# Kernel optimization log

Measured on AMD Instinct MI355X. Metric: run time of the kernel, lower is better.

The kernel has to match this reference:

```python
import jax, jax.numpy as jnp
import numpy as np

N = 3072      # atoms
C_A = 128     # atom channel
C_S = 384     # style/cond channel
C_Z = 16      # pair channel
H = 4         # heads
D = C_A // H  # head dim = 32
NEXP = 2      # FFN expansion
BIASINIT = -2.0


def _ln(x, eps=1e-5):
    m = x.mean(-1, keepdims=True)
    v = x.var(-1, keepdims=True)
    return (x - m) * jax.lax.rsqrt(v + eps)


def _adaln(a, s, s_w, scale_w, scale_b, shift_w):
    # AF3 Algorithm 26: a<-LN(a,no affine); s<-LN(s,no offset); a<-sigmoid(Lin(s))*a + LinNoBias(s)
    an = _ln(a)
    sn = _ln(s) * s_w
    return jax.nn.sigmoid(sn @ scale_w + scale_b) * an + sn @ shift_w


def setup_inputs() -> dict:
    key = jax.random.key(0)
    ks = iter(jax.random.split(key, 40))
    def w(shape, scale=0.02):
        return jax.random.normal(next(ks), shape, jnp.float32) * scale
    inp = dict(
        a=jax.random.normal(next(ks), (N, C_A), jnp.float32),
        s=jax.random.normal(next(ks), (N, C_S), jnp.float32),
        z=jax.random.normal(next(ks), (N, N, C_Z), jnp.float32),
        # AttentionPairBias: AdaLN params
        aln1_s_w=jnp.ones((C_S,), jnp.float32),
        aln1_scale_w=w((C_S, C_A)), aln1_scale_b=jnp.zeros((C_A,), jnp.float32),
        aln1_shift_w=w((C_S, C_A)),
        # attention projections
        wq=w((C_A, C_A)), bq=jnp.zeros((C_A,), jnp.float32),
        wk=w((C_A, C_A)), wv=w((C_A, C_A)),
        ln_z_w=jnp.ones((C_Z,), jnp.float32), ln_z_b=jnp.zeros((C_Z,), jnp.float32),
        wb=w((C_Z, H)),
        wg=w((C_A, C_A)), wo=w((C_A, C_A)),
        sgate1_w=w((C_S, C_A)), sgate1_b=jnp.full((C_A,), BIASINIT, jnp.float32),
        # ConditionedTransitionBlock: AdaLN params
        aln2_s_w=jnp.ones((C_S,), jnp.float32),
        aln2_scale_w=w((C_S, C_A)), aln2_scale_b=jnp.zeros((C_A,), jnp.float32),
        aln2_shift_w=w((C_S, C_A)),
        # SwiGLU FFN
        w1=w((C_A, NEXP * C_A)), w2=w((C_A, NEXP * C_A)), wout=w((NEXP * C_A, C_A)),
        sgate2_w=w((C_S, C_A)), sgate2_b=jnp.full((C_A,), BIASINIT, jnp.float32),
    )
    return inp


def reference(a, s, z,
              aln1_s_w, aln1_scale_w, aln1_scale_b, aln1_shift_w,
              wq, bq, wk, wv, ln_z_w, ln_z_b, wb, wg, wo, sgate1_w, sgate1_b,
              aln2_s_w, aln2_scale_w, aln2_scale_b, aln2_shift_w,
              w1, w2, wout, sgate2_w, sgate2_b):
    # ---- AttentionPairBias (Alg 24) ----
    h = _adaln(a, s, aln1_s_w, aln1_scale_w, aln1_scale_b, aln1_shift_w)
    q = (h @ wq + bq).reshape(N, H, D)
    k = (h @ wk).reshape(N, H, D)
    v = (h @ wv).reshape(N, H, D)
    # pair bias from layernormed z: [N, N, H]
    bias = (_ln(z) * ln_z_w + ln_z_b) @ wb
    logits = jnp.einsum('qhd,khd->hqk', q, k) / np.float32(np.sqrt(D)) + bias.transpose(2, 0, 1)
    attnw = jax.nn.softmax(logits, axis=-1)
    o = jnp.einsum('hqk,khd->qhd', attnw, v)
    g = jax.nn.sigmoid(h @ wg).reshape(N, H, D)
    attn = (g * o).reshape(N, C_A) @ wo
    attn = jax.nn.sigmoid(s @ sgate1_w + sgate1_b) * attn
    attn_out = attn + a  # residual 1
    # ---- ConditionedTransitionBlock (Alg 25) ----
    h2 = _adaln(attn_out, s, aln2_s_w, aln2_scale_w, aln2_scale_b, aln2_shift_w)
    gated = jax.nn.silu(h2 @ w1) * (h2 @ w2)  # SwiGLU, [N, 2*C_A]
    ff = jax.nn.sigmoid(s @ sgate2_w + sgate2_b) * (gated @ wout)
    out_a = ff + attn_out  # residual 2
    return out_a
```

## Files before the change

kernel.cpp:

```cpp
#include <hip/hip_runtime.h>
#include <math.h>

#define N_ATOMS 3072
#define C_Ac 128
#define C_Sc 384
#define C_Zc 16
#define QT 64
#define KC 16
#define CHUNK (N_ATOMS/KC)
#define KT 8
#define NST (CHUNK/KT)
#define NQT (N_ATOMS/QT)

__device__ __forceinline__ float sigm(float x){ return 1.f/(1.f+__expf(-x)); }

__global__ __launch_bounds__(256) void k_stage_a(
    const float* __restrict__ a, const float* __restrict__ s,
    const float* __restrict__ s_w, const float* __restrict__ scale_w,
    const float* __restrict__ scale_b, const float* __restrict__ shift_w,
    const float* __restrict__ wq, const float* __restrict__ bq,
    const float* __restrict__ wk, const float* __restrict__ wv,
    const float* __restrict__ wg,
    float* __restrict__ qo, float* __restrict__ ko, float* __restrict__ vo,
    float* __restrict__ go, float* __restrict__ lns)
{
  __shared__ float sn[4][C_Sc];
  __shared__ float an[4][C_Ac];
  __shared__ float hsh[4][C_Ac];
  __shared__ float t1[4][C_Ac], t2[4][C_Ac];
  int n0 = blockIdx.x*4;
  int tid = threadIdx.x, w = tid>>6, lane = tid&63;

  {
    const float* srow = s + (size_t)(n0+w)*C_Sc;
    float v[6]; float sx=0.f, sxx=0.f;
    #pragma unroll
    for (int j=0;j<6;j++){ v[j]=srow[lane+j*64]; sx+=v[j]; sxx+=v[j]*v[j]; }
    #pragma unroll
    for (int off=32;off;off>>=1){ sx+=__shfl_xor(sx,off,64); sxx+=__shfl_xor(sxx,off,64); }
    float mean=sx*(1.f/C_Sc), rs=rsqrtf(sxx*(1.f/C_Sc)-mean*mean+1e-5f);
    #pragma unroll
    for (int j=0;j<6;j++){
      int i=lane+j*64;
      float ln=(v[j]-mean)*rs;
      lns[(size_t)(n0+w)*C_Sc+i]=ln;
      sn[w][i]=ln*s_w[i];
    }
  }
  {
    const float* arow = a + (size_t)(n0+w)*C_Ac;
    float v0=arow[lane], v1=arow[lane+64];
    float sx=v0+v1, sxx=v0*v0+v1*v1;
    #pragma unroll
    for (int off=32;off;off>>=1){ sx+=__shfl_xor(sx,off,64); sxx+=__shfl_xor(sxx,off,64); }
    float mean=sx*(1.f/C_Ac), rs=rsqrtf(sxx*(1.f/C_Ac)-mean*mean+1e-5f);
    an[w][lane]=(v0-mean)*rs; an[w][lane+64]=(v1-mean)*rs;
  }
  __syncthreads();

  {
    int c = tid&127, sel = tid>>7;
    const float* W = sel ? shift_w : scale_w;
    float acc[4];
    #pragma unroll
    for (int r=0;r<4;r++) acc[r] = sel ? 0.f : scale_b[c];
    for (int i=0;i<C_Sc;i++){
      float wv = W[(size_t)i*C_Ac+c];
      #pragma unroll
      for (int r=0;r<4;r++) acc[r] += sn[r][i]*wv;
    }
    if (sel==0){ t1[0][c]=sigm(acc[0]); t1[1][c]=sigm(acc[1]); t1[2][c]=sigm(acc[2]); t1[3][c]=sigm(acc[3]); }
    else       { t2[0][c]=acc[0]; t2[1][c]=acc[1]; t2[2][c]=acc[2]; t2[3][c]=acc[3]; }
  }
  __syncthreads();
  for (int f=tid; f<512; f+=256){ int r=f>>7, c=f&127; hsh[r][c] = t1[r][c]*an[r][c] + t2[r][c]; }
  __syncthreads();

  {
    int c = tid&127, sel = tid>>7;
    const float* Wa = sel ? wv : wq;
    const float* Wb = sel ? wg : wk;
    float accA[4], accB[4];
    #pragma unroll
    for (int r=0;r<4;r++){ accA[r] = sel ? 0.f : bq[c]; accB[r]=0.f; }
    for (int i=0;i<C_Ac;i++){
      float wa=Wa[(size_t)i*C_Ac+c], wb_=Wb[(size_t)i*C_Ac+c];
      #pragma unroll
      for (int r=0;r<4;r++){ float hv=hsh[r][i]; accA[r]+=hv*wa; accB[r]+=hv*wb_; }
    }
    #pragma unroll
    for (int r=0;r<4;r++){
      size_t idx = (size_t)(n0+r)*C_Ac + c;
      if (sel==0){ qo[idx]=accA[r]; ko[idx]=accB[r]; }
      else       { vo[idx]=accA[r]; go[idx]=sigm(accB[r]); }
    }
  }
}

__global__ __launch_bounds__(256) void k_attn(
    const float* __restrict__ z, const float* __restrict__ ln_z_w,
    const float* __restrict__ ln_z_b, const float* __restrict__ wb,
    const float* __restrict__ qws, const float* __restrict__ kws,
    const float* __restrict__ vws,
    float* __restrict__ part_m, float* __restrict__ part_l,
    float* __restrict__ part_o)
{
  __shared__ float bias[4][QT][KT+1];
  __shared__ float ks[KT][C_Ac];
  __shared__ float vs[KT][C_Ac];
  __shared__ float lwb_s[C_Zc][4];
  __shared__ float csum_s[4], bb_s[4];

  int qt = blockIdx.x, chunk = blockIdx.y;
  int q0 = qt*QT, k_base = chunk*CHUNK;
  int tid = threadIdx.x, w = tid>>6, lane = tid&63;

  if (tid < 64){ int c = tid>>2, h = tid&3; lwb_s[c][h] = ln_z_w[c]*wb[c*4+h]; }
  if (tid < 4){
    float cs=0.f, bbv=0.f;
    #pragma unroll
    for (int c=0;c<C_Zc;c++){ cs += ln_z_w[c]*wb[c*4+tid]; bbv += ln_z_b[c]*wb[c*4+tid]; }
    csum_s[tid]=cs; bb_s[tid]=bbv;
  }
  __syncthreads();

  float qv[32];
  {
    const float4* qp = (const float4*)(qws + (size_t)(q0+lane)*C_Ac + w*32);
    #pragma unroll
    for (int j=0;j<8;j++){ float4 t=qp[j]; qv[4*j]=t.x; qv[4*j+1]=t.y; qv[4*j+2]=t.z; qv[4*j+3]=t.w; }
  }
  float m=-INFINITY, l=0.f, o[32];
  #pragma unroll
  for (int j=0;j<32;j++) o[j]=0.f;
  const float isd = 0.17677669529663687f;

  float z0[16], z1[16];
  float4 kreg, vreg;
  const int qla = (tid>>3), qlb = 32 + (tid>>3), klz = tid&7;

  {
    int k0n = k_base;
    const float4* zp0 = (const float4*)(z + ((size_t)(q0+qla)*N_ATOMS + (k0n+klz))*C_Zc);
    const float4* zp1 = (const float4*)(z + ((size_t)(q0+qlb)*N_ATOMS + (k0n+klz))*C_Zc);
    #pragma unroll
    for (int j=0;j<4;j++){ float4 t=zp0[j]; z0[4*j]=t.x; z0[4*j+1]=t.y; z0[4*j+2]=t.z; z0[4*j+3]=t.w; }
    #pragma unroll
    for (int j=0;j<4;j++){ float4 t=zp1[j]; z1[4*j]=t.x; z1[4*j+1]=t.y; z1[4*j+2]=t.z; z1[4*j+3]=t.w; }
    kreg = ((const float4*)(kws + (size_t)(k0n + (tid>>5))*C_Ac))[tid&31];
    vreg = ((const float4*)(vws + (size_t)(k0n + (tid>>5))*C_Ac))[tid&31];
  }

  #pragma unroll 1
  for (int st=0; st<NST; st++){
    ((float4*)ks)[tid] = kreg;
    ((float4*)vs)[tid] = vreg;
    {
      float sum=0.f, ssq=0.f;
      #pragma unroll
      for (int c=0;c<16;c++){ sum+=z0[c]; ssq+=z0[c]*z0[c]; }
      float mz=sum*(1.f/16), rz=rsqrtf(ssq*(1.f/16)-mz*mz+1e-5f);
      float d0=0.f,d1=0.f,d2=0.f,d3=0.f;
      #pragma unroll
      for (int c=0;c<16;c++){ float zc=z0[c];
        d0=fmaf(zc,lwb_s[c][0],d0); d1=fmaf(zc,lwb_s[c][1],d1);
        d2=fmaf(zc,lwb_s[c][2],d2); d3=fmaf(zc,lwb_s[c][3],d3); }
      bias[0][qla][klz]=rz*(d0-mz*csum_s[0])+bb_s[0];
      bias[1][qla][klz]=rz*(d1-mz*csum_s[1])+bb_s[1];
      bias[2][qla][klz]=rz*(d2-mz*csum_s[2])+bb_s[2];
      bias[3][qla][klz]=rz*(d3-mz*csum_s[3])+bb_s[3];
    }
    {
      float sum=0.f, ssq=0.f;
      #pragma unroll
      for (int c=0;c<16;c++){ sum+=z1[c]; ssq+=z1[c]*z1[c]; }
      float mz=sum*(1.f/16), rz=rsqrtf(ssq*(1.f/16)-mz*mz+1e-5f);
      float d0=0.f,d1=0.f,d2=0.f,d3=0.f;
      #pragma unroll
      for (int c=0;c<16;c++){ float zc=z1[c];
        d0=fmaf(zc,lwb_s[c][0],d0); d1=fmaf(zc,lwb_s[c][1],d1);
        d2=fmaf(zc,lwb_s[c][2],d2); d3=fmaf(zc,lwb_s[c][3],d3); }
      bias[0][qlb][klz]=rz*(d0-mz*csum_s[0])+bb_s[0];
      bias[1][qlb][klz]=rz*(d1-mz*csum_s[1])+bb_s[1];
      bias[2][qlb][klz]=rz*(d2-mz*csum_s[2])+bb_s[2];
      bias[3][qlb][klz]=rz*(d3-mz*csum_s[3])+bb_s[3];
    }
    if (st+1 < NST){
      int k0n = k_base + (st+1)*KT;
      const float4* zp0 = (const float4*)(z + ((size_t)(q0+qla)*N_ATOMS + (k0n+klz))*C_Zc);
      const float4* zp1 = (const float4*)(z + ((size_t)(q0+qlb)*N_ATOMS + (k0n+klz))*C_Zc);
      #pragma unroll
      for (int j=0;j<4;j++){ float4 t=zp0[j]; z0[4*j]=t.x; z0[4*j+1]=t.y; z0[4*j+2]=t.z; z0[4*j+3]=t.w; }
      #pragma unroll
      for (int j=0;j<4;j++){ float4 t=zp1[j]; z1[4*j]=t.x; z1[4*j+1]=t.y; z1[4*j+2]=t.z; z1[4*j+3]=t.w; }
      kreg = ((const float4*)(kws + (size_t)(k0n + (tid>>5))*C_Ac))[tid&31];
      vreg = ((const float4*)(vws + (size_t)(k0n + (tid>>5))*C_Ac))[tid&31];
    }
    asm volatile("s_waitcnt lgkmcnt(0)" ::: "memory");
    __builtin_amdgcn_s_barrier();
    float lg[KT];
    #pragma unroll
    for (int kl=0;kl<KT;kl++) lg[kl] = bias[w][lane][kl];
    #pragma unroll
    for (int kl=0;kl<KT;kl++){
      const float4* kp = (const float4*)&ks[kl][w*32];
      float d0=0.f,d1=0.f,d2=0.f,d3=0.f;
      #pragma unroll
      for (int j=0;j<8;j++){ float4 t=kp[j];
        d0=fmaf(qv[4*j],t.x,d0); d1=fmaf(qv[4*j+1],t.y,d1);
        d2=fmaf(qv[4*j+2],t.z,d2); d3=fmaf(qv[4*j+3],t.w,d3); }
      lg[kl] = fmaf((d0+d1)+(d2+d3), isd, lg[kl]);
    }
    float tm = fmaxf(fmaxf(fmaxf(lg[0],lg[1]),fmaxf(lg[2],lg[3])),
                     fmaxf(fmaxf(lg[4],lg[5]),fmaxf(lg[6],lg[7])));
    float mn = fmaxf(m, tm);
    float ef = __expf(m-mn);
    float ssum = 0.f;
    #pragma unroll
    for (int kl=0;kl<KT;kl++){ float e=__expf(lg[kl]-mn); lg[kl]=e; ssum+=e; }
    l = l*ef + ssum; m = mn;
    #pragma unroll
    for (int j=0;j<32;j++) o[j]*=ef;
    #pragma unroll
    for (int kl=0;kl<KT;kl++){
      const float4* vp = (const float4*)&vs[kl][w*32];
      float e = lg[kl];
      #pragma unroll
      for (int j=0;j<8;j++){ float4 t=vp[j];
        o[4*j]  =fmaf(e,t.x,o[4*j]);   o[4*j+1]=fmaf(e,t.y,o[4*j+1]);
        o[4*j+2]=fmaf(e,t.z,o[4*j+2]); o[4*j+3]=fmaf(e,t.w,o[4*j+3]); }
    }
    asm volatile("s_waitcnt lgkmcnt(0)" ::: "memory");
    __builtin_amdgcn_s_barrier();
  }

  size_t pb = (((size_t)chunk*NQT + qt)*4 + w)*64 + lane;
  part_m[pb]=m; part_l[pb]=l;
  float4* po = (float4*)(part_o + pb*32);
  #pragma unroll
  for (int j=0;j<8;j++){ po[j] = make_float4(o[4*j],o[4*j+1],o[4*j+2],o[4*j+3]); }
}

__global__ __launch_bounds__(256) void k_combine(
    const float* __restrict__ part_m, const float* __restrict__ part_l,
    const float* __restrict__ part_o, const float* __restrict__ gws,
    float* __restrict__ gows)
{
  int qt = blockIdx.x, h = blockIdx.y;
  int tid = threadIdx.x, ql = tid&63, dg = tid>>6;
  float mc[KC], lc[KC], M=-INFINITY;
  #pragma unroll
  for (int c=0;c<KC;c++){
    size_t pb = (((size_t)c*NQT + qt)*4 + h)*64 + ql;
    mc[c]=part_m[pb]; lc[c]=part_l[pb]; M=fmaxf(M,mc[c]);
  }
  float L=0.f, oa[8];
  #pragma unroll
  for (int j=0;j<8;j++) oa[j]=0.f;
  #pragma unroll
  for (int c=0;c<KC;c++){
    float sc=__expf(mc[c]-M);
    L += lc[c]*sc;
    const float4* po = (const float4*)(part_o + ((((size_t)c*NQT + qt)*4 + h)*64 + ql)*32 + dg*8);
    float4 t0=po[0], t1=po[1];
    oa[0]+=sc*t0.x; oa[1]+=sc*t0.y; oa[2]+=sc*t0.z; oa[3]+=sc*t0.w;
    oa[4]+=sc*t1.x; oa[5]+=sc*t1.y; oa[6]+=sc*t1.z; oa[7]+=sc*t1.w;
  }
  float invL = 1.f/L;
  size_t base = (size_t)(qt*64+ql)*C_Ac + h*32 + dg*8;
  #pragma unroll
  for (int j=0;j<8;j++) gows[base+j] = gws[base+j]*oa[j]*invL;
}

__global__ __launch_bounds__(256) void k_stage_c(
    const float* __restrict__ gows, const float* __restrict__ wo,
    const float* __restrict__ s, const float* __restrict__ sgate1_w,
    const float* __restrict__ sgate1_b, const float* __restrict__ a,
    const float* __restrict__ lns, const float* __restrict__ s_w2,
    const float* __restrict__ scale_w2, const float* __restrict__ scale_b2,
    const float* __restrict__ shift_w2, const float* __restrict__ w1,
    const float* __restrict__ w2, const float* __restrict__ wout,
    const float* __restrict__ sgate2_w, const float* __restrict__ sgate2_b,
    float* __restrict__ out)
{
  __shared__ float srow[4][C_Sc], sn2[4][C_Sc];
  __shared__ float gor[4][C_Ac], ats[4][C_Ac], h2[4][C_Ac];
  __shared__ float gated[4][2*C_Ac];
  __shared__ float t1[4][C_Ac], t2[4][C_Ac], ta[4][C_Ac], tb[4][C_Ac];
  int n0 = blockIdx.x*4;
  int tid = threadIdx.x, w = tid>>6, lane = tid&63;

  for (int r=0;r<4;r++)
    for (int i=tid;i<C_Sc;i+=256){
      float sv = s[(size_t)(n0+r)*C_Sc+i];
      srow[r][i]=sv;
      sn2[r][i]=lns[(size_t)(n0+r)*C_Sc+i]*s_w2[i];
    }
  for (int f=tid; f<512; f+=256){ int r=f>>7, c=f&127; gor[r][c]=gows[(size_t)(n0+r)*C_Ac+c]; }
  __syncthreads();

  {
    int c = tid&127, sel = tid>>7;
    float acc[4];
    if (sel==0){
      #pragma unroll
      for (int r=0;r<4;r++) acc[r]=0.f;
      for (int i=0;i<C_Ac;i++){
        float wv=wo[(size_t)i*C_Ac+c];
        #pragma unroll
        for (int r=0;r<4;r++) acc[r]+=gor[r][i]*wv;
      }
      #pragma unroll
      for (int r=0;r<4;r++) t1[r][c]=acc[r];
    } else {
      #pragma unroll
      for (int r=0;r<4;r++) acc[r]=sgate1_b[c];
      for (int i=0;i<C_Sc;i++){
        float wv=sgate1_w[(size_t)i*C_Ac+c];
        #pragma unroll
        for (int r=0;r<4;r++) acc[r]+=srow[r][i]*wv;
      }
      #pragma unroll
      for (int r=0;r<4;r++) t2[r][c]=sigm(acc[r]);
    }
  }
  __syncthreads();
  for (int f=tid; f<512; f+=256){ int r=f>>7, c=f&127;
    ats[r][c] = t2[r][c]*t1[r][c] + a[(size_t)(n0+r)*C_Ac+c]; }
  __syncthreads();

  {
    float v0=ats[w][lane], v1=ats[w][lane+64];
    float sx=v0+v1, sxx=v0*v0+v1*v1;
    #pragma unroll
    for (int off=32;off;off>>=1){ sx+=__shfl_xor(sx,off,64); sxx+=__shfl_xor(sxx,off,64); }
    float mean=sx*(1.f/C_Ac), rs=rsqrtf(sxx*(1.f/C_Ac)-mean*mean+1e-5f);
    t1[w][lane]=(v0-mean)*rs; t1[w][lane+64]=(v1-mean)*rs;
  }
  __syncthreads();

  {
    int c = tid&127, sel = tid>>7;
    float acc[4];
    const float* W = sel ? shift_w2 : scale_w2;
    #pragma unroll
    for (int r=0;r<4;r++) acc[r] = sel ? 0.f : scale_b2[c];
    for (int i=0;i<C_Sc;i++){
      float wv=W[(size_t)i*C_Ac+c];
      #pragma unroll
      for (int r=0;r<4;r++) acc[r]+=sn2[r][i]*wv;
    }
    if (sel==0){ 
      #pragma unroll
      for (int r=0;r<4;r++) ta[r][c]=sigm(acc[r])*t1[r][c];
    } else {
      #pragma unroll
      for (int r=0;r<4;r++) tb[r][c]=acc[r];
    }
  }
  __syncthreads();
  for (int f=tid; f<512; f+=256){ int r=f>>7, c=f&127; h2[r][c]=ta[r][c]+tb[r][c]; }
  __syncthreads();

  {
    int j = tid;
    float a1[4], a2[4];
    #pragma unroll
    for (int r=0;r<4;r++){ a1[r]=0.f; a2[r]=0.f; }
    for (int i=0;i<C_Ac;i++){
      float w1v=w1[(size_t)i*2*C_Ac+j], w2v=w2[(size_t)i*2*C_Ac+j];
      #pragma unroll
      for (int r=0;r<4;r++){ float hv=h2[r][i]; a1[r]+=hv*w1v; a2[r]+=hv*w2v; }
    }
    #pragma unroll
    for (int r=0;r<4;r++) gated[r][j]=a1[r]*sigm(a1[r])*a2[r];
  }
  __syncthreads();

  {
    int c = tid&127, sel = tid>>7;
    float acc[4];
    if (sel==0){
      #pragma unroll
      for (int r=0;r<4;r++) acc[r]=0.f;
      for (int j=0;j<2*C_Ac;j++){
        float wv=wout[(size_t)j*C_Ac+c];
        #pragma unroll
        for (int r=0;r<4;r++) acc[r]+=gated[r][j]*wv;
      }
      #pragma unroll
      for (int r=0;r<4;r++) t1[r][c]=acc[r];
    } else {
      #pragma unroll
      for (int r=0;r<4;r++) acc[r]=sgate2_b[c];
      for (int i=0;i<C_Sc;i++){
        float wv=sgate2_w[(size_t)i*C_Ac+c];
        #pragma unroll
        for (int r=0;r<4;r++) acc[r]+=srow[r][i]*wv;
      }
      #pragma unroll
      for (int r=0;r<4;r++) t2[r][c]=sigm(acc[r]);
    }
  }
  __syncthreads();
  for (int f=tid; f<512; f+=256){ int r=f>>7, c=f&127;
    out[(size_t)(n0+r)*C_Ac+c] = t2[r][c]*t1[r][c] + ats[r][c]; }
}

extern "C" void kernel_launch(void* const* d_in, const int* in_sizes, int n_in,
                              void* d_out, int out_size, void* d_ws, size_t ws_size,
                              hipStream_t stream)
{
  const float* a            = (const float*)d_in[0];
  const float* s            = (const float*)d_in[1];
  const float* z            = (const float*)d_in[2];
  const float* aln1_s_w     = (const float*)d_in[3];
  const float* aln1_scale_w = (const float*)d_in[4];
  const float* aln1_scale_b = (const float*)d_in[5];
  const float* aln1_shift_w = (const float*)d_in[6];
  const float* wq           = (const float*)d_in[7];
  const float* bq           = (const float*)d_in[8];
  const float* wk           = (const float*)d_in[9];
  const float* wv           = (const float*)d_in[10];
  const float* ln_z_w       = (const float*)d_in[11];
  const float* ln_z_b       = (const float*)d_in[12];
  const float* wb           = (const float*)d_in[13];
  const float* wg           = (const float*)d_in[14];
  const float* wo           = (const float*)d_in[15];
  const float* sgate1_w     = (const float*)d_in[16];
  const float* sgate1_b     = (const float*)d_in[17];
  const float* aln2_s_w     = (const float*)d_in[18];
  const float* aln2_scale_w = (const float*)d_in[19];
  const float* aln2_scale_b = (const float*)d_in[20];
  const float* aln2_shift_w = (const float*)d_in[21];
  const float* w1           = (const float*)d_in[22];
  const float* w2           = (const float*)d_in[23];
  const float* wout         = (const float*)d_in[24];
  const float* sgate2_w     = (const float*)d_in[25];
  const float* sgate2_b     = (const float*)d_in[26];
  float* out = (float*)d_out;

  float* ws   = (float*)d_ws;
  float* qws  = ws;
  float* kws  = qws  + (size_t)N_ATOMS*C_Ac;
  float* vws  = kws  + (size_t)N_ATOMS*C_Ac;
  float* gws  = vws  + (size_t)N_ATOMS*C_Ac;
  float* gows = gws  + (size_t)N_ATOMS*C_Ac;
  float* lns  = gows + (size_t)N_ATOMS*C_Ac;
  float* part_m = lns + (size_t)N_ATOMS*C_Sc;
  float* part_l = part_m + (size_t)KC*NQT*4*64;
  float* part_o = part_l + (size_t)KC*NQT*4*64;

  hipLaunchKernelGGL(k_stage_a, dim3(N_ATOMS/4), dim3(256), 0, stream,
      a, s, aln1_s_w, aln1_scale_w, aln1_scale_b, aln1_shift_w,
      wq, bq, wk, wv, wg, qws, kws, vws, gws, lns);
  hipLaunchKernelGGL(k_attn, dim3(NQT, KC), dim3(256), 0, stream,
      z, ln_z_w, ln_z_b, wb, qws, kws, vws, part_m, part_l, part_o);
  hipLaunchKernelGGL(k_combine, dim3(NQT, 4), dim3(256), 0, stream,
      part_m, part_l, part_o, gws, gows);
  hipLaunchKernelGGL(k_stage_c, dim3(N_ATOMS/4), dim3(256), 0, stream,
      gows, wo, s, sgate1_w, sgate1_b, a, lns, aln2_s_w,
      aln2_scale_w, aln2_scale_b, aln2_shift_w, w1, w2, wout,
      sgate2_w, sgate2_b, out);
}
```

Baseline: 1.108 ms.

## Process 8 rows per block in dense stages and double-buffer attention z prefetch

The pre- and post-attention dense kernels now handle 8 atoms per block instead of 4. Activations are stored transposed in shared memory so each step reads 8 values with float4 loads, which halves weight reloads per output row. The attention kernel gains a second register buffer for z/K/V, prefetching two tiles ahead to hide global load latency, at the cost of more registers and possibly lower occupancy. Stage C reuses one shared pool for all its buffers to keep LDS within limits.

```diff
diff --git a/kernel.cpp b/kernel.cpp
--- a/kernel.cpp
+++ b/kernel.cpp
@@ -24,15 +24,17 @@
     float* __restrict__ qo, float* __restrict__ ko, float* __restrict__ vo,
     float* __restrict__ go, float* __restrict__ lns)
 {
-  __shared__ float sn[4][C_Sc];
-  __shared__ float an[4][C_Ac];
-  __shared__ float hsh[4][C_Ac];
-  __shared__ float t1[4][C_Ac], t2[4][C_Ac];
-  int n0 = blockIdx.x*4;
+  __shared__ __align__(16) float snT[C_Sc][12];
+  __shared__ __align__(16) float an[8][C_Ac];
+  __shared__ __align__(16) float t1[8][C_Ac], t2[8][C_Ac];
+  __shared__ __align__(16) float hshT[C_Ac][12];
+  int n0 = blockIdx.x*8;
   int tid = threadIdx.x, w = tid>>6, lane = tid&63;
 
-  {
-    const float* srow = s + (size_t)(n0+w)*C_Sc;
+  #pragma unroll
+  for (int rr=0; rr<2; rr++){
+    int r = w + rr*4;
+    const float* srow = s + (size_t)(n0+r)*C_Sc;
     float v[6]; float sx=0.f, sxx=0.f;
     #pragma unroll
     for (int j=0;j<6;j++){ v[j]=srow[lane+j*64]; sx+=v[j]; sxx+=v[j]*v[j]; }
@@ -43,56 +45,79 @@
     for (int j=0;j<6;j++){
       int i=lane+j*64;
       float ln=(v[j]-mean)*rs;
-      lns[(size_t)(n0+w)*C_Sc+i]=ln;
-      sn[w][i]=ln*s_w[i];
-    }
-  }
-  {
-    const float* arow = a + (size_t)(n0+w)*C_Ac;
+      lns[(size_t)(n0+r)*C_Sc+i]=ln;
+      snT[i][r]=ln*s_w[i];
+    }
+  }
+  #pragma unroll
+  for (int rr=0; rr<2; rr++){
+    int r = w + rr*4;
+    const float* arow = a + (size_t)(n0+r)*C_Ac;
     float v0=arow[lane], v1=arow[lane+64];
     float sx=v0+v1, sxx=v0*v0+v1*v1;
     #pragma unroll
     for (int off=32;off;off>>=1){ sx+=__shfl_xor(sx,off,64); sxx+=__shfl_xor(sxx,off,64); }
     float mean=sx*(1.f/C_Ac), rs=rsqrtf(sxx*(1.f/C_Ac)-mean*mean+1e-5f);
-    an[w][lane]=(v0-mean)*rs; an[w][lane+64]=(v1-mean)*rs;
+    an[r][lane]=(v0-mean)*rs; an[r][lane+64]=(v1-mean)*rs;
   }
   __syncthreads();
 
   {
     int c = tid&127, sel = tid>>7;
     const float* W = sel ? shift_w : scale_w;
-    float acc[4];
-    #pragma unroll
-    for (int r=0;r<4;r++) acc[r] = sel ? 0.f : scale_b[c];
+    float acc[8];
+    float ini = sel ? 0.f : scale_b[c];
+    #pragma unroll
+    for (int r=0;r<8;r++) acc[r]=ini;
+    #pragma unroll 4
     for (int i=0;i<C_Sc;i++){
-      float wv = W[(size_t)i*C_Ac+c];
-      #pragma unroll
-      for (int r=0;r<4;r++) acc[r] += sn[r][i]*wv;
-    }
-    if (sel==0){ t1[0][c]=sigm(acc[0]); t1[1][c]=sigm(acc[1]); t1[2][c]=sigm(acc[2]); t1[3][c]=sigm(acc[3]); }
-    else       { t2[0][c]=acc[0]; t2[1][c]=acc[1]; t2[2][c]=acc[2]; t2[3][c]=acc[3]; }
-  }
-  __syncthreads();
-  for (int f=tid; f<512; f+=256){ int r=f>>7, c=f&127; hsh[r][c] = t1[r][c]*an[r][c] + t2[r][c]; }
-  __syncthreads();
-
-  {
-    int c = tid&127, sel = tid>>7;
-    const float* Wa = sel ? wv : wq;
-    const float* Wb = sel ? wg : wk;
-    float accA[4], accB[4];
-    #pragma unroll
-    for (int r=0;r<4;r++){ accA[r] = sel ? 0.f : bq[c]; accB[r]=0.f; }
+      float wv = W[i*C_Ac+c];
+      float4 s0 = *(const float4*)&snT[i][0];
+      float4 s1 = *(const float4*)&snT[i][4];
+      acc[0]=fmaf(s0.x,wv,acc[0]); acc[1]=fmaf(s0.y,wv,acc[1]);
+      acc[2]=fmaf(s0.z,wv,acc[2]); acc[3]=fmaf(s0.w,wv,acc[3]);
+      acc[4]=fmaf(s1.x,wv,acc[4]); acc[5]=fmaf(s1.y,wv,acc[5]);
+      acc[6]=fmaf(s1.z,wv,acc[6]); acc[7]=fmaf(s1.w,wv,acc[7]);
+    }
+    if (sel==0){
+      #pragma unroll
+      for (int r=0;r<8;r++) t1[r][c]=sigm(acc[r]);
+    } else {
+      #pragma unroll
+      for (int r=0;r<8;r++) t2[r][c]=acc[r];
+    }
+  }
+  __syncthreads();
+  for (int f=tid; f<8*C_Ac; f+=256){ int r=f>>7, c=f&127; hshT[c][r] = t1[r][c]*an[r][c] + t2[r][c]; }
+  __syncthreads();
+
+  {
+    int c = tid&127, selA = tid>>7;
+    const float* WA = selA ? wk : wq;
+    const float* WB = selA ? wg : wv;
+    float accA[8], accB[8];
+    float ini = selA ? 0.f : bq[c];
+    #pragma unroll
+    for (int r=0;r<8;r++){ accA[r]=ini; accB[r]=0.f; }
+    #pragma unroll 4
     for (int i=0;i<C_Ac;i++){
-      float wa=Wa[(size_t)i*C_Ac+c], wb_=Wb[(size_t)i*C_Ac+c];
-      #pragma unroll
-      for (int r=0;r<4;r++){ float hv=hsh[r][i]; accA[r]+=hv*wa; accB[r]+=hv*wb_; }
-    }
-    #pragma unroll
-    for (int r=0;r<4;r++){
+      float wa=WA[i*C_Ac+c], wb_=WB[i*C_Ac+c];
+      float4 h0 = *(const float4*)&hshT[i][0];
+      float4 h1 = *(const float4*)&hshT[i][4];
+      accA[0]=fmaf(h0.x,wa,accA[0]); accA[1]=fmaf(h0.y,wa,accA[1]);
+      accA[2]=fmaf(h0.z,wa,accA[2]); accA[3]=fmaf(h0.w,wa,accA[3]);
+      accA[4]=fmaf(h1.x,wa,accA[4]); accA[5]=fmaf(h1.y,wa,accA[5]);
+      accA[6]=fmaf(h1.z,wa,accA[6]); accA[7]=fmaf(h1.w,wa,accA[7]);
+      accB[0]=fmaf(h0.x,wb_,accB[0]); accB[1]=fmaf(h0.y,wb_,accB[1]);
+      accB[2]=fmaf(h0.z,wb_,accB[2]); accB[3]=fmaf(h0.w,wb_,accB[3]);
+      accB[4]=fmaf(h1.x,wb_,accB[4]); accB[5]=fmaf(h1.y,wb_,accB[5]);
+      accB[6]=fmaf(h1.z,wb_,accB[6]); accB[7]=fmaf(h1.w,wb_,accB[7]);
+    }
+    #pragma unroll
+    for (int r=0;r<8;r++){
       size_t idx = (size_t)(n0+r)*C_Ac + c;
-      if (sel==0){ qo[idx]=accA[r]; ko[idx]=accB[r]; }
-      else       { vo[idx]=accA[r]; go[idx]=sigm(accB[r]); }
+      if (selA==0){ qo[idx]=accA[r]; vo[idx]=accB[r]; }
+      else        { ko[idx]=accA[r]; go[idx]=sigm(accB[r]); }
     }
   }
 }
@@ -105,9 +130,9 @@
     float* __restrict__ part_m, float* __restrict__ part_l,
     float* __restrict__ part_o)
 {
-  __shared__ float bias[4][QT][KT+1];
-  __shared__ float ks[KT][C_Ac];
-  __shared__ float vs[KT][C_Ac];
+  __shared__ __align__(16) float bias[4][QT][KT+1];
+  __shared__ __align__(16) float ks[KT][C_Ac];
+  __shared__ __align__(16) float vs[KT][C_Ac];
   __shared__ float lwb_s[C_Zc][4];
   __shared__ float csum_s[4], bb_s[4];
 
@@ -135,103 +160,78 @@
   for (int j=0;j<32;j++) o[j]=0.f;
   const float isd = 0.17677669529663687f;
 
-  float z0[16], z1[16];
-  float4 kreg, vreg;
   const int qla = (tid>>3), qlb = 32 + (tid>>3), klz = tid&7;
 
-  {
-    int k0n = k_base;
-    const float4* zp0 = (const float4*)(z + ((size_t)(q0+qla)*N_ATOMS + (k0n+klz))*C_Zc);
-    const float4* zp1 = (const float4*)(z + ((size_t)(q0+qlb)*N_ATOMS + (k0n+klz))*C_Zc);
-    #pragma unroll
-    for (int j=0;j<4;j++){ float4 t=zp0[j]; z0[4*j]=t.x; z0[4*j+1]=t.y; z0[4*j+2]=t.z; z0[4*j+3]=t.w; }
-    #pragma unroll
-    for (int j=0;j<4;j++){ float4 t=zp1[j]; z1[4*j]=t.x; z1[4*j+1]=t.y; z1[4*j+2]=t.z; z1[4*j+3]=t.w; }
-    kreg = ((const float4*)(kws + (size_t)(k0n + (tid>>5))*C_Ac))[tid&31];
-    vreg = ((const float4*)(vws + (size_t)(k0n + (tid>>5))*C_Ac))[tid&31];
-  }
+  float z0A[16], z1A[16], z0B[16], z1B[16];
+  float4 kregA, vregA, kregB, vregB;
+
+#define LOADBUF(Z0, Z1, KR, VR, K0N)                                          \
+  { int k0n = (K0N);                                                          \
+    const float4* zp0 = (const float4*)(z + ((size_t)(q0+qla)*N_ATOMS + (k0n+klz))*C_Zc); \
+    const float4* zp1 = (const float4*)(z + ((size_t)(q0+qlb)*N_ATOMS + (k0n+klz))*C_Zc); \
+    _Pragma("unroll") for (int j=0;j<4;j++){ float4 t=zp0[j]; Z0[4*j]=t.x; Z0[4*j+1]=t.y; Z0[4*j+2]=t.z; Z0[4*j+3]=t.w; } \
+    _Pragma("unroll") for (int j=0;j<4;j++){ float4 t=zp1[j]; Z1[4*j]=t.x; Z1[4*j+1]=t.y; Z1[4*j+2]=t.z; Z1[4*j+3]=t.w; } \
+    KR = ((const float4*)(kws + (size_t)(k0n + (tid>>5))*C_Ac))[tid&31];      \
+    VR = ((const float4*)(vws + (size_t)(k0n + (tid>>5))*C_Ac))[tid&31]; }
+
+#define BIAS_PAIR(ZZ, QL)                                                     \
+  { float sum=0.f, ssq=0.f;                                                   \
+    _Pragma("unroll") for (int c=0;c<16;c++){ sum+=ZZ[c]; ssq+=ZZ[c]*ZZ[c]; } \
+    float mz=sum*(1.f/16), rz=rsqrtf(ssq*(1.f/16)-mz*mz+1e-5f);               \
+    float d0=0.f,d1=0.f,d2=0.f,d3=0.f;                                        \
+    _Pragma("unroll") for (int c=0;c<16;c++){ float zc=ZZ[c];                 \
+      d0=fmaf(zc,lwb_s[c][0],d0); d1=fmaf(zc,lwb_s[c][1],d1);                 \
+      d2=fmaf(zc,lwb_s[c][2],d2); d3=fmaf(zc,lwb_s[c][3],d3); }               \
+    bias[0][QL][klz]=rz*(d0-mz*csum_s[0])+bb_s[0];                            \
+    bias[1][QL][klz]=rz*(d1-mz*csum_s[1])+bb_s[1];                            \
+    bias[2][QL][klz]=rz*(d2-mz*csum_s[2])+bb_s[2];                            \
+    bias[3][QL][klz]=rz*(d3-mz*csum_s[3])+bb_s[3]; }
+
+#define MAIN_TILE()                                                           \
+  { float lg[KT];                                                             \
+    _Pragma("unroll") for (int kl=0;kl<KT;kl++) lg[kl] = bias[w][lane][kl];   \
+    _Pragma("unroll") for (int kl=0;kl<KT;kl++){                              \
+      const float4* kp = (const float4*)&ks[kl][w*32];                        \
+      float d0=0.f,d1=0.f,d2=0.f,d3=0.f;                                      \
+      _Pragma("unroll") for (int j=0;j<8;j++){ float4 t=kp[j];                \
+        d0=fmaf(qv[4*j],t.x,d0); d1=fmaf(qv[4*j+1],t.y,d1);                   \
+        d2=fmaf(qv[4*j+2],t.z,d2); d3=fmaf(qv[4*j+3],t.w,d3); }               \
+      lg[kl] = fmaf((d0+d1)+(d2+d3), isd, lg[kl]);                            \
+    }                                                                         \
+    float tm = fmaxf(fmaxf(fmaxf(lg[0],lg[1]),fmaxf(lg[2],lg[3])),            \
+                     fmaxf(fmaxf(lg[4],lg[5]),fmaxf(lg[6],lg[7])));           \
+    float mn = fmaxf(m, tm);                                                  \
+    float ef = __expf(m-mn);                                                  \
+    float ssum = 0.f;                                                         \
+    _Pragma("unroll") for (int kl=0;kl<KT;kl++){ float e=__expf(lg[kl]-mn); lg[kl]=e; ssum+=e; } \
+    l = l*ef + ssum; m = mn;                                                  \
+    _Pragma("unroll") for (int j=0;j<32;j++) o[j]*=ef;                        \
+    _Pragma("unroll") for (int kl=0;kl<KT;kl++){                              \
+      const float4* vp = (const float4*)&vs[kl][w*32];                        \
+      float e = lg[kl];                                                       \
+      _Pragma("unroll") for (int j=0;j<8;j++){ float4 t=vp[j];                \
+        o[4*j]  =fmaf(e,t.x,o[4*j]);   o[4*j+1]=fmaf(e,t.y,o[4*j+1]);         \
+        o[4*j+2]=fmaf(e,t.z,o[4*j+2]); o[4*j+3]=fmaf(e,t.w,o[4*j+3]); } } }
+
+#define ROUND(Z0, Z1, KR, VR, ST)                                             \
+  { ((float4*)ks)[tid] = KR;                                                  \
+    ((float4*)vs)[tid] = VR;                                                  \
+    BIAS_PAIR(Z0, qla);                                                       \
+    BIAS_PAIR(Z1, qlb);                                                       \
+    if ((ST)+2 < NST){ LOADBUF(Z0, Z1, KR, VR, k_base + ((ST)+2)*KT); }       \
+    asm volatile("s_waitcnt lgkmcnt(0)" ::: "memory");                        \
+    __builtin_amdgcn_s_barrier();                                             \
+    MAIN_TILE();                                                              \
+    asm volatile("s_waitcnt lgkmcnt(0)" ::: "memory");                        \
+    __builtin_amdgcn_s_barrier(); }
+
+  LOADBUF(z0A, z1A, kregA, vregA, k_base);
+  LOADBUF(z0B, z1B, kregB, vregB, k_base + KT);
 
   #pragma unroll 1
-  for (int st=0; st<NST; st++){
-    ((float4*)ks)[tid] = kreg;
-    ((float4*)vs)[tid] = vreg;
-    {
-      float sum=0.f, ssq=0.f;
-      #pragma unroll
-      for (int c=0;c<16;c++){ sum+=z0[c]; ssq+=z0[c]*z0[c]; }
-      float mz=sum*(1.f/16), rz=rsqrtf(ssq*(1.f/16)-mz*mz+1e-5f);
-      float d0=0.f,d1=0.f,d2=0.f,d3=0.f;
-      #pragma unroll
-      for (int c=0;c<16;c++){ float zc=z0[c];
-        d0=fmaf(zc,lwb_s[c][0],d0); d1=fmaf(zc,lwb_s[c][1],d1);
-        d2=fmaf(zc,lwb_s[c][2],d2); d3=fmaf(zc,lwb_s[c][3],d3); }
-      bias[0][qla][klz]=rz*(d0-mz*csum_s[0])+bb_s[0];
-      bias[1][qla][klz]=rz*(d1-mz*csum_s[1])+bb_s[1];
-      bias[2][qla][klz]=rz*(d2-mz*csum_s[2])+bb_s[2];
-      bias[3][qla][klz]=rz*(d3-mz*csum_s[3])+bb_s[3];
-    }
-    {
-      float sum=0.f, ssq=0.f;
-      #pragma unroll
-      for (int c=0;c<16;c++){ sum+=z1[c]; ssq+=z1[c]*z1[c]; }
-      float mz=sum*(1.f/16), rz=rsqrtf(ssq*(1.f/16)-mz*mz+1e-5f);
-      float d0=0.f,d1=0.f,d2=0.f,d3=0.f;
-      #pragma unroll
-      for (int c=0;c<16;c++){ float zc=z1[c];
-        d0=fmaf(zc,lwb_s[c][0],d0); d1=fmaf(zc,lwb_s[c][1],d1);
-        d2=fmaf(zc,lwb_s[c][2],d2); d3=fmaf(zc,lwb_s[c][3],d3); }
-      bias[0][qlb][klz]=rz*(d0-mz*csum_s[0])+bb_s[0];
-      bias[1][qlb][klz]=rz*(d1-mz*csum_s[1])+bb_s[1];
-      bias[2][qlb][klz]=rz*(d2-mz*csum_s[2])+bb_s[2];
-      bias[3][qlb][klz]=rz*(d3-mz*csum_s[3])+bb_s[3];
-    }
-    if (st+1 < NST){
-      int k0n = k_base + (st+1)*KT;
-      const float4* zp0 = (const float4*)(z + ((size_t)(q0+qla)*N_ATOMS + (k0n+klz))*C_Zc);
-      const float4* zp1 = (const float4*)(z + ((size_t)(q0+qlb)*N_ATOMS + (k0n+klz))*C_Zc);
-      #pragma unroll
-      for (int j=0;j<4;j++){ float4 t=zp0[j]; z0[4*j]=t.x; z0[4*j+1]=t.y; z0[4*j+2]=t.z; z0[4*j+3]=t.w; }
-      #pragma unroll
-      for (int j=0;j<4;j++){ float4 t=zp1[j]; z1[4*j]=t.x; z1[4*j+1]=t.y; z1[4*j+2]=t.z; z1[4*j+3]=t.w; }
-      kreg = ((const float4*)(kws + (size_t)(k0n + (tid>>5))*C_Ac))[tid&31];
-      vreg = ((const float4*)(vws + (size_t)(k0n + (tid>>5))*C_Ac))[tid&31];
-    }
-    asm volatile("s_waitcnt lgkmcnt(0)" ::: "memory");
-    __builtin_amdgcn_s_barrier();
-    float lg[KT];
-    #pragma unroll
-    for (int kl=0;kl<KT;kl++) lg[kl] = bias[w][lane][kl];
-    #pragma unroll
-    for (int kl=0;kl<KT;kl++){
-      const float4* kp = (const float4*)&ks[kl][w*32];
-      float d0=0.f,d1=0.f,d2=0.f,d3=0.f;
-      #pragma unroll
-      for (int j=0;j<8;j++){ float4 t=kp[j];
-        d0=fmaf(qv[4*j],t.x,d0); d1=fmaf(qv[4*j+1],t.y,d1);
-        d2=fmaf(qv[4*j+2],t.z,d2); d3=fmaf(qv[4*j+3],t.w,d3); }
-      lg[kl] = fmaf((d0+d1)+(d2+d3), isd, lg[kl]);
-    }
-    float tm = fmaxf(fmaxf(fmaxf(lg[0],lg[1]),fmaxf(lg[2],lg[3])),
-                     fmaxf(fmaxf(lg[4],lg[5]),fmaxf(lg[6],lg[7])));
-    float mn = fmaxf(m, tm);
-    float ef = __expf(m-mn);
-    float ssum = 0.f;
-    #pragma unroll
-    for (int kl=0;kl<KT;kl++){ float e=__expf(lg[kl]-mn); lg[kl]=e; ssum+=e; }
-    l = l*ef + ssum; m = mn;
-    #pragma unroll
-    for (int j=0;j<32;j++) o[j]*=ef;
-    #pragma unroll
-    for (int kl=0;kl<KT;kl++){
-      const float4* vp = (const float4*)&vs[kl][w*32];
-      float e = lg[kl];
-      #pragma unroll
-      for (int j=0;j<8;j++){ float4 t=vp[j];
-        o[4*j]  =fmaf(e,t.x,o[4*j]);   o[4*j+1]=fmaf(e,t.y,o[4*j+1]);
-        o[4*j+2]=fmaf(e,t.z,o[4*j+2]); o[4*j+3]=fmaf(e,t.w,o[4*j+3]); }
-    }
-    asm volatile("s_waitcnt lgkmcnt(0)" ::: "memory");
-    __builtin_amdgcn_s_barrier();
+  for (int st=0; st<NST; st+=2){
+    ROUND(z0A, z1A, kregA, vregA, st);
+    ROUND(z0B, z1B, kregB, vregB, st+1);
   }
 
   size_t pb = (((size_t)chunk*NQT + qt)*4 + w)*64 + lane;
@@ -239,6 +239,10 @@
   float4* po = (float4*)(part_o + pb*32);
   #pragma unroll
   for (int j=0;j<8;j++){ po[j] = make_float4(o[4*j],o[4*j+1],o[4*j+2],o[4*j+3]); }
+#undef ROUND
+#undef MAIN_TILE
+#undef BIAS_PAIR
+#undef LOADBUF
 }
 
 __global__ __launch_bounds__(256) void k_combine(
@@ -283,128 +287,174 @@
     const float* __restrict__ sgate2_w, const float* __restrict__ sgate2_b,
     float* __restrict__ out)
 {
-  __shared__ float srow[4][C_Sc], sn2[4][C_Sc];
-  __shared__ float gor[4][C_Ac], ats[4][C_Ac], h2[4][C_Ac];
-  __shared__ float gated[4][2*C_Ac];
-  __shared__ float t1[4][C_Ac], t2[4][C_Ac], ta[4][C_Ac], tb[4][C_Ac];
-  int n0 = blockIdx.x*4;
+  __shared__ __align__(16) float POOL[16384];
+#define sT(i,r)     POOL[(i)*12+(r)]
+#define sn2T(i,r)   POOL[4608+(i)*12+(r)]
+#define gatedT(i,r) POOL[4608+(i)*12+(r)]
+#define gorT(i,r)   POOL[9216+(i)*12+(r)]
+#define tbM(r,c)    POOL[9216+(r)*C_Ac+(c)]
+#define atsM(r,c)   POOL[10752+(r)*C_Ac+(c)]
+#define anvM(r,c)   POOL[11776+(r)*C_Ac+(c)]
+#define t1M(r,c)    POOL[12800+(r)*C_Ac+(c)]
+#define t2M(r,c)    POOL[13824+(r)*C_Ac+(c)]
+#define h2T(i,r)    POOL[14848+(i)*12+(r)]
+  int n0 = blockIdx.x*8;
   int tid = threadIdx.x, w = tid>>6, lane = tid&63;
 
-  for (int r=0;r<4;r++)
+  for (int r=0;r<8;r++)
     for (int i=tid;i<C_Sc;i+=256){
-      float sv = s[(size_t)(n0+r)*C_Sc+i];
-      srow[r][i]=sv;
-      sn2[r][i]=lns[(size_t)(n0+r)*C_Sc+i]*s_w2[i];
-    }
-  for (int f=tid; f<512; f+=256){ int r=f>>7, c=f&127; gor[r][c]=gows[(size_t)(n0+r)*C_Ac+c]; }
+      sT(i,r)   = s[(size_t)(n0+r)*C_Sc+i];
+      sn2T(i,r) = lns[(size_t)(n0+r)*C_Sc+i]*s_w2[i];
+    }
+  for (int f=tid; f<8*C_Ac; f+=256){ int r=f>>7, c=f&127; gorT(c,r)=gows[(size_t)(n0+r)*C_Ac+c]; }
   __syncthreads();
 
   {
     int c = tid&127, sel = tid>>7;
-    float acc[4];
+    float acc[8];
     if (sel==0){
       #pragma unroll
-      for (int r=0;r<4;r++) acc[r]=0.f;
+      for (int r=0;r<8;r++) acc[r]=0.f;
+      #pragma unroll 4
       for (int i=0;i<C_Ac;i++){
-        float wv=wo[(size_t)i*C_Ac+c];
-        #pragma unroll
-        for (int r=0;r<4;r++) acc[r]+=gor[r][i]*wv;
+        float wv=wo[i*C_Ac+c];
+        float4 g0=*(const float4*)&gorT(i,0), g1=*(const float4*)&gorT(i,4);
+        acc[0]=fmaf(g0.x,wv,acc[0]); acc[1]=fmaf(g0.y,wv,acc[1]);
+        acc[2]=fmaf(g0.z,wv,acc[2]); acc[3]=fmaf(g0.w,wv,acc[3]);
+        acc[4]=fmaf(g1.x,wv,acc[4]); acc[5]=fmaf(g1.y,wv,acc[5]);
+        acc[6]=fmaf(g1.z,wv,acc[6]); acc[7]=fmaf(g1.w,wv,acc[7]);
       }
       #pragma unroll
-      for (int r=0;r<4;r++) t1[r][c]=acc[r];
+      for (int r=0;r<8;r++) t1M(r,c)=acc[r];
     } else {
       #pragma unroll
-      for (int r=0;r<4;r++) acc[r]=sgate1_b[c];
+      for (int r=0;r<8;r++) acc[r]=sgate1_b[c];
+      #pragma unroll 4
       for (int i=0;i<C_Sc;i++){
-        float wv=sgate1_w[(size_t)i*C_Ac+c];
-        #pragma unroll
-        for (int r=0;r<4;r++) acc[r]+=srow[r][i]*wv;
+        float wv=sgate1_w[i*C_Ac+c];
+        float4 s0=*(const float4*)&sT(i,0), s1=*(const float4*)&sT(i,4);
+        acc[0]=fmaf(s0.x,wv,acc[0]); acc[1]=fmaf(s0.y,wv,acc[1]);
+        acc[2]=fmaf(s0.z,wv,acc[2]); acc[3]=fmaf(s0.w,wv,acc[3]);
+        acc[4]=fmaf(s1.x,wv,acc[4]); acc[5]=fmaf(s1.y,wv,acc[5]);
+        acc[6]=fmaf(s1.z,wv,acc[6]); acc[7]=fmaf(s1.w,wv,acc[7]);
       }
       #pragma unroll
-      for (int r=0;r<4;r++) t2[r][c]=sigm(acc[r]);
-    }
-  }
-  __syncthreads();
-  for (int f=tid; f<512; f+=256){ int r=f>>7, c=f&127;
-    ats[r][c] = t2[r][c]*t1[r][c] + a[(size_t)(n0+r)*C_Ac+c]; }
-  __syncthreads();
-
-  {
-    float v0=ats[w][lane], v1=ats[w][lane+64];
+      for (int r=0;r<8;r++) t2M(r,c)=sigm(acc[r]);
+    }
+  }
+  __syncthreads();
+  for (int f=tid; f<8*C_Ac; f+=256){ int r=f>>7, c=f&127;
+    atsM(r,c) = t2M(r,c)*t1M(r,c) + a[(size_t)(n0+r)*C_Ac+c]; }
+  __syncthreads();
+
+  #pragma unroll
+  for (int rr=0; rr<2; rr++){
+    int r = w + rr*4;
+    float v0=atsM(r,lane), v1=atsM(r,lane+64);
     float sx=v0+v1, sxx=v0*v0+v1*v1;
     #pragma unroll
     for (int off=32;off;off>>=1){ sx+=__shfl_xor(sx,off,64); sxx+=__shfl_xor(sxx,off,64); }
     float mean=sx*(1.f/C_Ac), rs=rsqrtf(sxx*(1.f/C_Ac)-mean*mean+1e-5f);
-    t1[w][lane]=(v0-mean)*rs; t1[w][lane+64]=(v1-mean)*rs;
+    anvM(r,lane)=(v0-mean)*rs; anvM(r,lane+64)=(v1-mean)*rs;
   }
   __syncthreads();
 
   {
     int c = tid&127, sel = tid>>7;
-    float acc[4];
     const float* W = sel ? shift_w2 : scale_w2;
-    #pragma unroll
-    for (int r=0;r<4;r++) acc[r] = sel ? 0.f : scale_b2[c];
+    float acc[8];
+    float ini = sel ? 0.f : scale_b2[c];
+    #pragma unroll
+    for (int r=0;r<8;r++) acc[r]=ini;
+    #pragma unroll 4
     for (int i=0;i<C_Sc;i++){
-      float wv=W[(size_t)i*C_Ac+c];
-      #pragma unroll
-      for (int r=0;r<4;r++) acc[r]+=sn2[r][i]*wv;
-    }
-    if (sel==0){ 
-      #pragma unroll
-      for (int r=0;r<4;r++) ta[r][c]=sigm(acc[r])*t1[r][c];
+      float wv=W[i*C_Ac+c];
+      float4 s0=*(const float4*)&sn2T(i,0), s1=*(const float4*)&sn2T(i,4);
+      acc[0]=fmaf(s0.x,wv,acc[0]); acc[1]=fmaf(s0.y,wv,acc[1]);
+      acc[2]=fmaf(s0.z,wv,acc[2]); acc[3]=fmaf(s0.w,wv,acc[3]);
+      acc[4]=fmaf(s1.x,wv,acc[4]); acc[5]=fmaf(s1.y,wv,acc[5]);
+      acc[6]=fmaf(s1.z,wv,acc[6]); acc[7]=fmaf(s1.w,wv,acc[7]);
+    }
+    if (sel==0){
+      #pragma unroll
+      for (int r=0;r<8;r++) t2M(r,c)=sigm(acc[r])*anvM(r,c);
     } else {
       #pragma unroll
-      for (int r=0;r<4;r++) tb[r][c]=acc[r];
-    }
-  }
-  __syncthreads();
-  for (int f=tid; f<512; f+=256){ int r=f>>7, c=f&127; h2[r][c]=ta[r][c]+tb[r][c]; }
-  __syncthreads();
-
-  {
-    int j = tid;
-    float a1[4], a2[4];
-    #pragma unroll
-    for (int r=0;r<4;r++){ a1[r]=0.f; a2[r]=0.f; }
+      for (int r=0;r<8;r++) tbM(r,c)=acc[r];
+    }
+  }
+  __syncthreads();
+  for (int f=tid; f<8*C_Ac; f+=256){ int r=f>>7, c=f&127; h2T(c,r)=t2M(r,c)+tbM(r,c); }
+  __syncthreads();
+
+  {
+    float a1[8], a2[8];
+    #pragma unroll
+    for (int r=0;r<8;r++){ a1[r]=0.f; a2[r]=0.f; }
+    #pragma unroll 2
     for (int i=0;i<C_Ac;i++){
-      float w1v=w1[(size_t)i*2*C_Ac+j], w2v=w2[(size_t)i*2*C_Ac+j];
-      #pragma unroll
-      for (int r=0;r<4;r++){ float hv=h2[r][i]; a1[r]+=hv*w1v; a2[r]+=hv*w2v; }
-    }
-    #pragma unroll
-    for (int r=0;r<4;r++) gated[r][j]=a1[r]*sigm(a1[r])*a2[r];
+      float w1v=w1[i*2*C_Ac+tid], w2v=w2[i*2*C_Ac+tid];
+      float4 h0=*(const float4*)&h2T(i,0), h1=*(const float4*)&h2T(i,4);
+      a1[0]=fmaf(h0.x,w1v,a1[0]); a1[1]=fmaf(h0.y,w1v,a1[1]);
+      a1[2]=fmaf(h0.z,w1v,a1[2]); a1[3]=fmaf(h0.w,w1v,a1[3]);
+      a1[4]=fmaf(h1.x,w1v,a1[4]); a1[5]=fmaf(h1.y,w1v,a1[5]);
+      a1[6]=fmaf(h1.z,w1v,a1[6]); a1[7]=fmaf(h1.w,w1v,a1[7]);
+      a2[0]=fmaf(h0.x,w2v,a2[0]); a2[1]=fmaf(h0.y,w2v,a2[1]);
+      a2[2]=fmaf(h0.z,w2v,a2[2]); a2[3]=fmaf(h0.w,w2v,a2[3]);
+      a2[4]=fmaf(h1.x,w2v,a2[4]); a2[5]=fmaf(h1.y,w2v,a2[5]);
+      a2[6]=fmaf(h1.z,w2v,a2[6]); a2[7]=fmaf(h1.w,w2v,a2[7]);
+    }
+    #pragma unroll
+    for (int r=0;r<8;r++) gatedT(tid,r)=a1[r]*sigm(a1[r])*a2[r];
   }
   __syncthreads();
 
   {
     int c = tid&127, sel = tid>>7;
-    float acc[4];
+    float acc[8];
     if (sel==0){
       #pragma unroll
-      for (int r=0;r<4;r++) acc[r]=0.f;
-      for (int j=0;j<2*C_Ac;j++){
-        float wv=wout[(size_t)j*C_Ac+c];
-        #pragma unroll
-        for (int r=0;r<4;r++) acc[r]+=gated[r][j]*wv;
+      for (int r=0;r<8;r++) acc[r]=0.f;
+      #pragma unroll 4
+      for (int i=0;i<2*C_Ac;i++){
+        float wv=wout[i*C_Ac+c];
+        float4 g0=*(const float4*)&gatedT(i,0), g1=*(const float4*)&gatedT(i,4);
+        acc[0]=fmaf(g0.x,wv,acc[0]); acc[1]=fmaf(g0.y,wv,acc[1]);
+        acc[2]=fmaf(g0.z,wv,acc[2]); acc[3]=fmaf(g0.w,wv,acc[3]);
+        acc[4]=fmaf(g1.x,wv,acc[4]); acc[5]=fmaf(g1.y,wv,acc[5]);
+        acc[6]=fmaf(g1.z,wv,acc[6]); acc[7]=fmaf(g1.w,wv,acc[7]);
       }
       #pragma unroll
-      for (int r=0;r<4;r++) t1[r][c]=acc[r];
+      for (int r=0;r<8;r++) t1M(r,c)=acc[r];
     } else {
       #pragma unroll
-      for (int r=0;r<4;r++) acc[r]=sgate2_b[c];
+      for (int r=0;r<8;r++) acc[r]=sgate2_b[c];
+      #pragma unroll 4
       for (int i=0;i<C_Sc;i++){
-        float wv=sgate2_w[(size_t)i*C_Ac+c];
-        #pragma unroll
-        for (int r=0;r<4;r++) acc[r]+=srow[r][i]*wv;
+        float wv=sgate2_w[i*C_Ac+c];
+        float4 s0=*(const float4*)&sT(i,0), s1=*(const float4*)&sT(i,4);
+        acc[0]=fmaf(s0.x,wv,acc[0]); acc[1]=fmaf(s0.y,wv,acc[1]);
+        acc[2]=fmaf(s0.z,wv,acc[2]); acc[3]=fmaf(s0.w,wv,acc[3]);
+        acc[4]=fmaf(s1.x,wv,acc[4]); acc[5]=fmaf(s1.y,wv,acc[5]);
+        acc[6]=fmaf(s1.z,wv,acc[6]); acc[7]=fmaf(s1.w,wv,acc[7]);
       }
       #pragma unroll
-      for (int r=0;r<4;r++) t2[r][c]=sigm(acc[r]);
-    }
-  }
-  __syncthreads();
-  for (int f=tid; f<512; f+=256){ int r=f>>7, c=f&127;
-    out[(size_t)(n0+r)*C_Ac+c] = t2[r][c]*t1[r][c] + ats[r][c]; }
+      for (int r=0;r<8;r++) t2M(r,c)=sigm(acc[r]);
+    }
+  }
+  __syncthreads();
+  for (int f=tid; f<8*C_Ac; f+=256){ int r=f>>7, c=f&127;
+    out[(size_t)(n0+r)*C_Ac+c] = t2M(r,c)*t1M(r,c) + atsM(r,c); }
+#undef sT
+#undef sn2T
+#undef gatedT
+#undef gorT
+#undef tbM
+#undef atsM
+#undef anvM
+#undef t1M
+#undef t2M
+#undef h2T
 }
 
 extern "C" void kernel_launch(void* const* d_in, const int* in_sizes, int n_in,
@@ -451,14 +501,14 @@
   float* part_l = part_m + (size_t)KC*NQT*4*64;
   float* part_o = part_l + (size_t)KC*NQT*4*64;
 
-  hipLaunchKernelGGL(k_stage_a, dim3(N_ATOMS/4), dim3(256), 0, stream,
+  hipLaunchKernelGGL(k_stage_a, dim3(N_ATOMS/8), dim3(256), 0, stream,
       a, s, aln1_s_w, aln1_scale_w, aln1_scale_b, aln1_shift_w,
       wq, bq, wk, wv, wg, qws, kws, vws, gws, lns);
   hipLaunchKernelGGL(k_attn, dim3(NQT, KC), dim3(256), 0, stream,
       z, ln_z_w, ln_z_b, wb, qws, kws, vws, part_m, part_l, part_o);
   hipLaunchKernelGGL(k_combine, dim3(NQT, 4), dim3(256), 0, stream,
       part_m, part_l, part_o, gws, gows);
-  hipLaunchKernelGGL(k_stage_c, dim3(N_ATOMS/4), dim3(256), 0, stream,
+  hipLaunchKernelGGL(k_stage_c, dim3(N_ATOMS/8), dim3(256), 0, stream,
       gows, wo, s, sgate1_w, sgate1_b, a, lns, aln2_s_w,
       aln2_scale_w, aln2_scale_b, aln2_shift_w, w1, w2, wout,
       sgate2_w, sgate2_b, out);
```

Result: slower. 2.232 ms (+101.6%).
